# Optimization experiments

Hardware: AMD Instinct MI355X
Metric: run time of the kernel (lower is better)

## Reference

```python
import jax, jax.numpy as jnp
import numpy as np
from jax import lax

D = 8          # conv_out_size
HID = 128      # lstm hidden
EMB = 32       # word embed
GD = 256       # g/f mlp width


def _coords():
    # faithful to cvt_coord with python3 float division on first component
    c = np.zeros((D * D, 2), dtype=np.float32)
    for i in range(D * D):
        c[i, 0] = (i / D - D / 2) / (D / 2.0)
        c[i, 1] = (i % D - D / 2) / (D / 2.0)
    return jnp.asarray(c)


def _conv_bn(x, k, b, gamma, beta):
    y = lax.conv_general_dilated(x, k, (2, 2), [(1, 1), (1, 1)],
                                 dimension_numbers=('NCHW', 'OIHW', 'NCHW'))
    y = jax.nn.relu(y + b[None, :, None, None])
    m = y.mean((0, 2, 3))
    v = ((y - m[None, :, None, None]) ** 2).mean((0, 2, 3))  # biased var (train-mode BN)
    y = (y - m[None, :, None, None]) * lax.rsqrt(v + 1e-5)[None, :, None, None]
    return gamma[None, :, None, None] * y + beta[None, :, None, None]


def setup_inputs() -> dict:
    key = jax.random.key(0)
    ks = iter(jax.random.split(key, 48))
    B, T, QV, AV = 64, 18, 90, 28
    n = lambda sh, s=0.1: jax.random.normal(next(ks), sh, jnp.float32) * s
    inp = {
        'img': jax.random.normal(next(ks), (B, 3, 128, 128), jnp.float32),
        'qst_idxs': jax.random.randint(next(ks), (B, T), 0, QV),
        'emb': n((QV, EMB)).at[0].set(0.0),  # padding_idx=0
        'W_ih': n((4 * HID, EMB)), 'W_hh': n((4 * HID, HID)),
        'b_ih': n((4 * HID,)), 'b_hh': n((4 * HID,)),
        'k1': n((24, 3, 3, 3)), 'cb1': n((24,)), 'g1': jnp.ones((24,)), 'be1': jnp.zeros((24,)),
        'k2': n((24, 24, 3, 3)), 'cb2': n((24,)), 'g2': jnp.ones((24,)), 'be2': jnp.zeros((24,)),
        'k3': n((24, 24, 3, 3)), 'cb3': n((24,)), 'g3': jnp.ones((24,)), 'be3': jnp.zeros((24,)),
        'k4': n((24, 24, 3, 3)), 'cb4': n((24,)), 'g4': jnp.ones((24,)), 'be4': jnp.zeros((24,)),
        'Wg1': n((GD, 180)), 'bg1': n((GD,)),
        'Wg2': n((GD, GD)), 'bg2': n((GD,)),
        'Wg3': n((GD, GD)), 'bg3': n((GD,)),
        'Wg4': n((GD, GD)), 'bg4': n((GD,)),
        'Wf1': n((GD, GD)), 'bf1': n((GD,)),
        'Wf2': n((GD, GD)), 'bf2': n((GD,)),
        'Wf3': n((AV, GD)), 'bf3': n((AV,)),
        'h0': jax.random.normal(next(ks), (B, HID), jnp.float32),
        'c0': jax.random.normal(next(ks), (B, HID), jnp.float32),
    }
    return inp


def reference(img, qst_idxs, emb, W_ih, W_hh, b_ih, b_hh,
              k1, cb1, g1, be1, k2, cb2, g2, be2, k3, cb3, g3, be3, k4, cb4, g4, be4,
              Wg1, bg1, Wg2, bg2, Wg3, bg3, Wg4, bg4,
              Wf1, bf1, Wf2, bf2, Wf3, bf3, h0, c0):
    B = img.shape[0]
    # --- question encoder: embedding (padding_idx=0) + LSTM, take final CELL state ---
    we = emb[qst_idxs] * (qst_idxs != 0)[..., None].astype(emb.dtype)  # [B,T,32]

    def step(carry, x_t):
        h, c = carry
        gates = x_t @ W_ih.T + h @ W_hh.T + (b_ih + b_hh)
        i, f, g, o = jnp.split(gates, 4, axis=-1)
        c = jax.nn.sigmoid(f) * c + jax.nn.sigmoid(i) * jnp.tanh(g)
        h = jax.nn.sigmoid(o) * jnp.tanh(c)
        return (h, c), None

    (h_n, c_n), _ = lax.scan(step, (h0, c0), we.transpose(1, 0, 2))
    qst = c_n  # original uses self.hidden[1][-1] == cell state, [B,128]

    # --- conv stack ---
    x = _conv_bn(img, k1, cb1, g1, be1)
    x = _conv_bn(x, k2, cb2, g2, be2)
    x = _conv_bn(x, k3, cb3, g3, be3)
    x = _conv_bn(x, k4, cb4, g4, be4)  # [B,24,8,8]

    xf = x.reshape(B, 24, D * D).transpose(0, 2, 1)            # [B,64,24]
    xf = jnp.concatenate([xf, jnp.broadcast_to(_coords(), (B, D * D, 2))], 2)  # [B,64,26]

    # --- g-MLP over all pairs; first linear decomposed across x_i / x_j / qst ---
    # pair (k,j) feature = [x_flat[j](26), x_flat[k](26), qst(128)]
    Ai = xf @ Wg1[:, :26].T                    # [B,64,256], x_i part (index j)
    Aj = xf @ Wg1[:, 26:52].T                  # [B,64,256], x_j part (index k)
    Q = qst @ Wg1[:, 52:].T + bg1              # [B,256]
    h = jax.nn.relu(Ai[:, None, :, :] + Aj[:, :, None, :] + Q[:, None, None, :])  # [B,64,64,256]
    h = jax.nn.relu(h @ Wg2.T + bg2)
    h = jax.nn.relu(h @ Wg3.T + bg3)
    h = jax.nn.relu(h @ Wg4.T + bg4)
    xg = h.sum((1, 2))                          # [B,256] sum-pool over pairs

    # --- f-MLP (dropout = identity in eval) ---
    xfc = jax.nn.relu(xg @ Wf1.T + bf1)
    xfc = jax.nn.relu(xfc @ Wf2.T + bf2)
    logits = xfc @ Wf3.T + bf3
    return jax.nn.log_softmax(logits, axis=-1)
```

## Files before the change

### kernel.cpp

```cpp
#include <hip/hip_runtime.h>
#include <math.h>

typedef __bf16 bf16x8 __attribute__((ext_vector_type(8)));
typedef float  f32x16 __attribute__((ext_vector_type(16)));

#define DEVFN __device__ __forceinline__

DEVFN unsigned short f2bfh(float f) {
    __bf16 h = (__bf16)f;
    union { __bf16 h; unsigned short u; } v; v.h = h;
    return v.u;
}
DEVFN float sigmoidf_(float x) { return 1.0f / (1.0f + expf(-x)); }

__global__ void lstm_cvt_kernel(const int* __restrict__ qidx, const float* __restrict__ emb,
                                const float* __restrict__ Wih, const float* __restrict__ Whh,
                                const float* __restrict__ bih, const float* __restrict__ bhh,
                                const float* __restrict__ h0, const float* __restrict__ c0,
                                float* __restrict__ qst,
                                const float* __restrict__ Wg2, const float* __restrict__ Wg3,
                                const float* __restrict__ Wg4,
                                unsigned short* __restrict__ Wt2, unsigned short* __restrict__ Wt3,
                                unsigned short* __restrict__ Wt4)
{
    int tid = threadIdx.x;
    if (blockIdx.x >= 64) {
        int i = (blockIdx.x - 64) * 512 + tid;
        int seg = i >> 16, idx = i & 65535;
        const float* src = (seg == 0) ? Wg2 : (seg == 1) ? Wg3 : Wg4;
        unsigned short* dst = (seg == 0) ? Wt2 : (seg == 1) ? Wt3 : Wt4;
        int col = idx >> 8, k = idx & 255;
        dst[(k >> 3)*2048 + col*8 + (k & 7)] = f2bfh(src[idx]);
        return;
    }
    int b = blockIdx.x;
    __shared__ float hs[128], cs[128], xs[32], gs[512];
    if (tid < 128) { hs[tid] = h0[b*128 + tid]; cs[tid] = c0[b*128 + tid]; }
    float bsum = bih[tid] + bhh[tid];
    for (int t = 0; t < 18; ++t) {
        if (tid < 32) {
            int id = qidx[b*18 + t];
            xs[tid] = (id != 0) ? emb[id*32 + tid] : 0.0f;
        }
        __syncthreads();
        float g = bsum;
        const float* wi = Wih + tid*32;
        #pragma unroll
        for (int d = 0; d < 32; ++d) g += xs[d] * wi[d];
        const float* wh = Whh + tid*128;
        for (int d = 0; d < 128; ++d) g += hs[d] * wh[d];
        gs[tid] = g;
        __syncthreads();
        if (tid < 128) {
            float ig = sigmoidf_(gs[tid]);
            float fg = sigmoidf_(gs[128 + tid]);
            float gg = tanhf(gs[256 + tid]);
            float og = sigmoidf_(gs[384 + tid]);
            float cn = fg * cs[tid] + ig * gg;
            cs[tid] = cn;
            hs[tid] = og * tanhf(cn);
        }
        __syncthreads();
    }
    if (tid < 128) qst[b*128 + tid] = cs[tid];
}

__launch_bounds__(256, 4)
__global__ void conv1_kernel(const float* __restrict__ img, const float* __restrict__ wk,
                             const float* __restrict__ cb, float* __restrict__ y1)
{
    __shared__ float simg[3][9][128];
    __shared__ __align__(16) float wl[3][9][24];
    __shared__ float cbs[24];
    int b = blockIdx.x, t = blockIdx.y, tid = threadIdx.x;
    for (int i = tid; i < 648; i += 256) {
        int co = i / 27, rem = i % 27;
        wl[rem / 9][rem % 9][co] = wk[i];
    }
    if (tid < 24) cbs[tid] = cb[tid];
    int base = 8*t - 1;
    for (int i = tid; i < 3*9*128; i += 256) {
        int ci = i / (9*128); int r2 = i % (9*128);
        int row = r2 / 128, colx = r2 % 128;
        int ih = base + row;
        simg[ci][row][colx] = (ih >= 0 && ih < 128) ?
            img[((size_t)(b*3 + ci)*128 + ih)*128 + colx] : 0.f;
    }
    __syncthreads();

    int ow = tid & 63;
    int os = tid >> 6;
    int oh = t*4 + os;
    float* yb = y1 + ((size_t)b*24*64 + oh)*64 + ow;

    #pragma unroll
    for (int co4 = 0; co4 < 24; co4 += 4) {
        float a0 = 0.f, a1 = 0.f, a2 = 0.f, a3 = 0.f;
        #pragma unroll
        for (int ci = 0; ci < 3; ++ci)
          #pragma unroll
          for (int kh = 0; kh < 3; ++kh)
            #pragma unroll
            for (int kw = 0; kw < 3; ++kw) {
                int iw = ow*2 + kw - 1;
                float x = (iw >= 0 && iw < 128) ? simg[ci][2*os + kh][iw] : 0.f;
                float4 w4 = *reinterpret_cast<const float4*>(&wl[ci][kh*3 + kw][co4]);
                a0 += x*w4.x; a1 += x*w4.y; a2 += x*w4.z; a3 += x*w4.w;
            }
        yb[(size_t)(co4+0)*4096] = fmaxf(a0 + cbs[co4+0], 0.f);
        yb[(size_t)(co4+1)*4096] = fmaxf(a1 + cbs[co4+1], 0.f);
        yb[(size_t)(co4+2)*4096] = fmaxf(a2 + cbs[co4+2], 0.f);
        yb[(size_t)(co4+3)*4096] = fmaxf(a3 + cbs[co4+3], 0.f);
    }
}

__global__ void bn_partial_kernel(const float* __restrict__ y, float* __restrict__ part,
                                  int HW, int nb)
{
    int c = blockIdx.x;
    int s = blockIdx.y;
    int S = gridDim.y;
    int tid = threadIdx.x;
    int n4 = HW >> 2;
    float sum = 0.f, sum2 = 0.f;
    for (int b = s * nb; b < (s + 1) * nb; ++b) {
        const float4* p = reinterpret_cast<const float4*>(y + ((size_t)(b*24 + c)) * HW);
        for (int i = tid; i < n4; i += 256) {
            float4 v = p[i];
            sum  += v.x + v.y + v.z + v.w;
            sum2 += v.x*v.x + v.y*v.y + v.z*v.z + v.w*v.w;
        }
    }
    __shared__ float rs[256], rs2[256];
    rs[tid] = sum; rs2[tid] = sum2;
    __syncthreads();
    for (int st = 128; st > 0; st >>= 1) {
        if (tid < st) { rs[tid] += rs[tid + st]; rs2[tid] += rs2[tid + st]; }
        __syncthreads();
    }
    if (tid == 0) {
        part[(c * S + s) * 2]     = rs[0];
        part[(c * S + s) * 2 + 1] = rs2[0];
    }
}

#define BN_FOLD(bnp, gamma, beta, S, N, abs_, abo_, tid)                    \
    if (tid < 24) {                                                          \
        float s_ = 0.f, s2_ = 0.f;                                           \
        for (int i_ = 0; i_ < (S); ++i_) {                                   \
            s_  += (bnp)[((tid)*(S) + i_)*2];                                \
            s2_ += (bnp)[((tid)*(S) + i_)*2 + 1];                            \
        }                                                                    \
        float m_ = s_ / (N);                                                 \
        float v_ = s2_ / (N) - m_*m_;                                        \
        float r_ = rsqrtf(v_ + 1e-5f);                                       \
        float a_ = (gamma)[tid] * r_;                                        \
        (abs_)[tid] = a_; (abo_)[tid] = (beta)[tid] - m_*a_;                 \
    }

__launch_bounds__(128, 4)
__global__ void conv2_kernel(const float* __restrict__ y1, const float* __restrict__ wk,
                             const float* __restrict__ cb,
                             const float* __restrict__ bnp, const float* __restrict__ gamma,
                             const float* __restrict__ beta,
                             float* __restrict__ y2)
{
    __shared__ float sin2[24][5][64];
    __shared__ float wl[24][9][24];
    __shared__ float cbs[24];
    __shared__ float abs_[24], abo_[24];
    int b = blockIdx.x, t = blockIdx.y, tid = threadIdx.x;
    BN_FOLD(bnp, gamma, beta, 16, 262144, abs_, abo_, tid);
    for (int i = tid; i < 5184; i += 128) {
        int co = i / 216, rem = i % 216;
        int ci = rem / 9, tap = rem % 9;
        wl[ci][tap][co] = wk[i];
    }
    if (tid < 24) cbs[tid] = cb[tid];
    __syncthreads();
    int base = 4*t - 1;
    for (int i = tid; i < 24*5*64; i += 128) {
        int ci = i / (5*64); int r2 = i % (5*64);
        int row = r2 / 64, colx = r2 % 64;
        int ih = base + row;
        sin2[ci][row][colx] = (ih >= 0 && ih < 64) ?
            y1[((size_t)(b*24 + ci)*64 + ih)*64 + colx] * abs_[ci] + abo_[ci] : 0.f;
    }
    __syncthreads();

    int pos = tid & 63;
    int ow = pos & 31, os = pos >> 5;
    int ch = tid >> 6;
    int oh = 2*t + os;
    float acc[12];
    #pragma unroll
    for (int c = 0; c < 12; ++c) acc[c] = 0.f;

    for (int ci = 0; ci < 24; ++ci) {
        #pragma unroll
        for (int kh = 0; kh < 3; ++kh)
          #pragma unroll
          for (int kw = 0; kw < 3; ++kw) {
            int iw = ow*2 + kw - 1;
            float x = (iw >= 0 && iw < 64) ? sin2[ci][2*os + kh][iw] : 0.f;
            const float* wv = &wl[ci][kh*3 + kw][ch*12];
            #pragma unroll
            for (int c4 = 0; c4 < 3; ++c4) {
                float4 w4 = *reinterpret_cast<const float4*>(wv + c4*4);
                acc[c4*4+0] += x*w4.x;
                acc[c4*4+1] += x*w4.y;
                acc[c4*4+2] += x*w4.z;
                acc[c4*4+3] += x*w4.w;
            }
          }
    }
    #pragma unroll
    for (int c = 0; c < 12; ++c) {
        int co = ch*12 + c;
        y2[((size_t)(b*24 + co)*32 + oh)*32 + ow] = fmaxf(acc[c] + cbs[co], 0.f);
    }
}

__launch_bounds__(256, 2)
__global__ void conv_kernel(const float* __restrict__ in, const float* __restrict__ wk,
                            const float* __restrict__ cb,
                            const float* __restrict__ bnp, const float* __restrict__ gamma,
                            const float* __restrict__ beta, int S, int N,
                            float* __restrict__ out,
                            int Cin, int Hin, int Win, int Hout, int Wout)
{
    int cob = blockIdx.x;
    int co = cob % 24, b = cob / 24;
    int tid = threadIdx.x;
    __shared__ float sw[24*9];
    __shared__ float so9[9];
    __shared__ float bias;
    __shared__ float abs_[24], abo_[24];
    BN_FOLD(bnp, gamma, beta, S, N, abs_, abo_, tid);
    __syncthreads();
    if (tid < Cin*9) {
        int ci = tid / 9, t = tid % 9;
        sw[tid] = wk[(co*Cin + ci)*9 + t] * abs_[ci];
    }
    if (tid < 9) {
        float s = 0.f;
        for (int ci = 0; ci < Cin; ++ci)
            s += abo_[ci] * wk[(co*Cin + ci)*9 + tid];
        so9[tid] = s;
    }
    if (tid == 0) bias = cb[co];
    __syncthreads();

    int HW = Hout * Wout;
    int pos = tid;
    if (pos >= HW) return;
    int ow = pos % Wout, oh = pos / Wout;

    float acc = bias;
    #pragma unroll
    for (int kh = 0; kh < 3; ++kh) {
        int ih = oh*2 + kh - 1;
        bool vh = (ih >= 0 && ih < Hin);
        #pragma unroll
        for (int kw = 0; kw < 3; ++kw) {
            int iw = ow*2 + kw - 1;
            if (vh && iw >= 0 && iw < Win) acc += so9[kh*3 + kw];
        }
    }
    const float* ipb = in + ((size_t)b * Cin) * Hin * Win;
    for (int ci = 0; ci < Cin; ++ci) {
        const float* ip = ipb + (size_t)ci * Hin * Win;
        const float* swp = sw + ci*9;
        #pragma unroll
        for (int kh = 0; kh < 3; ++kh) {
            int ih = oh*2 + kh - 1;
            if (ih < 0 || ih >= Hin) continue;
            #pragma unroll
            for (int kw = 0; kw < 3; ++kw) {
                int iw = ow*2 + kw - 1;
                if (iw < 0 || iw >= Win) continue;
                acc += ip[ih*Win + iw] * swp[kh*3 + kw];
            }
        }
    }
    out[((size_t)(b*24 + co)) * HW + pos] = fmaxf(acc, 0.0f);
}

__global__ void aiajq_kernel(const float* __restrict__ y4,
                             const float* __restrict__ bnp, const float* __restrict__ gamma,
                             const float* __restrict__ beta,
                             const float* __restrict__ qst,
                             const float* __restrict__ Wg1, const float* __restrict__ bg1,
                             float* __restrict__ Ai, float* __restrict__ Aj, float* __restrict__ Q)
{
    int b = blockIdx.x, c = threadIdx.x;
    __shared__ float xfl[64 * 26];
    __shared__ float qv[128];
    __shared__ float abs_[24], abo_[24];
    BN_FOLD(bnp, gamma, beta, 1, 4096, abs_, abo_, c);
    __syncthreads();
    for (int i = c; i < 64*24; i += 256) {
        int p = i / 24, ch = i % 24;
        xfl[p*26 + ch] = y4[((size_t)(b*24 + ch)) * 64 + p] * abs_[ch] + abo_[ch];
    }
    if (c < 64) {
        xfl[c*26 + 24] = ((float)c / 8.0f - 4.0f) * 0.25f;
        xfl[c*26 + 25] = ((float)(c % 8) - 4.0f) * 0.25f;
    }
    if (c < 128) qv[c] = qst[b*128 + c];
    __syncthreads();
    const float* w = Wg1 + (size_t)c * 180;
    float wa[26], wb[26];
    #pragma unroll
    for (int d = 0; d < 26; ++d) { wa[d] = w[d]; wb[d] = w[26 + d]; }
    float q = bg1[c];
    for (int d = 0; d < 128; ++d) q += qv[d] * w[52 + d];
    Q[b*256 + c] = q;
    for (int j = 0; j < 64; ++j) {
        const float* xr = xfl + j*26;
        float sa = 0.f, sb = 0.f;
        #pragma unroll
        for (int d = 0; d < 26; ++d) { sa += xr[d]*wa[d]; sb += xr[d]*wb[d]; }
        Ai[((size_t)(b*64 + j))*256 + c] = sa;
        Aj[((size_t)(b*64 + j))*256 + c] = sb;
    }
}

__launch_bounds__(512, 4)
__global__ void gmlp_kernel(const float* __restrict__ Ai, const float* __restrict__ Aj,
                            const float* __restrict__ Q,
                            const unsigned short* __restrict__ Wt2, const float* __restrict__ bg2,
                            const unsigned short* __restrict__ Wt3, const float* __restrict__ bg3,
                            const unsigned short* __restrict__ Wt4, const float* __restrict__ bg4,
                            float* __restrict__ partial)
{
    constexpr int LDP = 264;
    __shared__ __align__(16) unsigned short buf[128 * LDP];
    int tid = threadIdx.x;
    int blk = blockIdx.x;
    int b = blk >> 5;
    int k0 = (blk & 31) << 1;

    {
        int g  = tid >> 8;
        int jh = (tid >> 7) & 1;
        int c2 = tid & 127;
        float2 aj = *((const float2*)(Aj + ((size_t)(b*64 + k0 + g))*256) + c2);
        float2 qq = *((const float2*)(Q + b*256) + c2);
        float a0 = aj.x + qq.x, a1 = aj.y + qq.y;
        const float2* aip = (const float2*)(Ai + ((size_t)b*64)*256) + c2;
        #pragma unroll 4
        for (int j = jh*32; j < jh*32 + 32; ++j) {
            float2 av = aip[(size_t)j*128];
            unsigned lo = f2bfh(fmaxf(av.x + a0, 0.f));
            unsigned hv = f2bfh(fmaxf(av.y + a1, 0.f));
            *(unsigned*)(&buf[(size_t)(g*64 + j)*LDP + 2*c2]) = lo | (hv << 16);
        }
    }
    __syncthreads();

    int l = tid & 63, w = tid >> 6;
    int rh = w >> 2;
    int cg = w & 3;
    int lid = l & 31, hi = l >> 5;
    int arow = rh*64 + lid;
    int colA = cg*64 + lid;
    int colB = colA + 32;

    const unsigned short* Ws[3] = {Wt2, Wt3, Wt4};
    const float* Bs[3] = {bg2, bg3, bg4};

    #pragma unroll
    for (int layer = 0; layer < 3; ++layer) {
        const unsigned short* W = Ws[layer];
        const float* bias = Bs[layer];
        f32x16 acc00, acc01, acc10, acc11;
        #pragma unroll
        for (int i = 0; i < 16; ++i) { acc00[i]=0.f; acc01[i]=0.f; acc10[i]=0.f; acc11[i]=0.f; }

        const unsigned short* wp0 = W + (size_t)hi*2048 + colA*8;
        const unsigned short* wp1 = W + (size_t)hi*2048 + colB*8;
        const unsigned short* ap  = buf + arow*LDP + hi*8;

        #pragma unroll
        for (int kk = 0; kk < 16; ++kk) {
            bf16x8 b0 = *reinterpret_cast<const bf16x8*>(wp0 + kk*4096);
            bf16x8 b1 = *reinterpret_cast<const bf16x8*>(wp1 + kk*4096);
            bf16x8 a0 = *reinterpret_cast<const bf16x8*>(ap + kk*16);
            bf16x8 a1 = *reinterpret_cast<const bf16x8*>(ap + 32*LDP + kk*16);
            acc00 = __builtin_amdgcn_mfma_f32_32x32x16_bf16(a0, b0, acc00, 0, 0, 0);
            acc01 = __builtin_amdgcn_mfma_f32_32x32x16_bf16(a0, b1, acc01, 0, 0, 0);
            acc10 = __builtin_amdgcn_mfma_f32_32x32x16_bf16(a1, b0, acc10, 0, 0, 0);
            acc11 = __builtin_amdgcn_mfma_f32_32x32x16_bf16(a1, b1, acc11, 0, 0, 0);
        }

        if (layer < 2) {
            float bc0 = bias[colA], bc1 = bias[colB];
            __syncthreads();
            #pragma unroll
            for (int reg = 0; reg < 16; ++reg) {
                int r0 = rh*64 + (reg & 3) + 8*(reg >> 2) + 4*hi;
                buf[r0*LDP + colA] = f2bfh(fmaxf(acc00[reg] + bc0, 0.f));
                buf[r0*LDP + colB] = f2bfh(fmaxf(acc01[reg] + bc1, 0.f));
                int r1 = r0 + 32;
                buf[r1*LDP + colA] = f2bfh(fmaxf(acc10[reg] + bc0, 0.f));
                buf[r1*LDP + colB] = f2bfh(fmaxf(acc11[reg] + bc1, 0.f));
            }
            __syncthreads();
        } else {
            float bc0 = bias[colA], bc1 = bias[colB];
            float cs0 = 0.f, cs1 = 0.f;
            #pragma unroll
            for (int reg = 0; reg < 16; ++reg) {
                cs0 += fmaxf(acc00[reg] + bc0, 0.f) + fmaxf(acc10[reg] + bc0, 0.f);
                cs1 += fmaxf(acc01[reg] + bc1, 0.f) + fmaxf(acc11[reg] + bc1, 0.f);
            }
            cs0 += __shfl_xor(cs0, 32);
            cs1 += __shfl_xor(cs1, 32);
            if (hi == 0) {
                float* pp = partial + ((size_t)blk*2 + rh)*256;
                pp[colA] = cs0;
                pp[colB] = cs1;
            }
        }
    }
}

__global__ void fmlp_kernel(const float* __restrict__ partial,
                            const float* __restrict__ Wf1, const float* __restrict__ bf1,
                            const float* __restrict__ Wf2, const float* __restrict__ bf2,
                            const float* __restrict__ Wf3, const float* __restrict__ bf3,
                            float* __restrict__ out)
{
    int b = blockIdx.x, tid = threadIdx.x;
    __shared__ float v0[256], v1[256], lgt[28];
    {
        float s0 = 0.f, s1 = 0.f, s2 = 0.f, s3 = 0.f;
        const float* p = partial + ((size_t)b * 64) * 256 + tid;
        #pragma unroll
        for (int k = 0; k < 64; k += 4) {
            s0 += p[(size_t)(k+0) * 256];
            s1 += p[(size_t)(k+1) * 256];
            s2 += p[(size_t)(k+2) * 256];
            s3 += p[(size_t)(k+3) * 256];
        }
        v0[tid] = (s0 + s1) + (s2 + s3);
    }
    __syncthreads();
    {
        float s = bf1[tid];
        const float4* wr = reinterpret_cast<const float4*>(Wf1 + (size_t)tid * 256);
        for (int k4 = 0; k4 < 64; ++k4) {
            float4 wv = wr[k4];
            s += wv.x*v0[k4*4+0] + wv.y*v0[k4*4+1] + wv.z*v0[k4*4+2] + wv.w*v0[k4*4+3];
        }
        v1[tid] = fmaxf(s, 0.f);
    }
    __syncthreads();
    {
        float s = bf2[tid];
        const float4* wr = reinterpret_cast<const float4*>(Wf2 + (size_t)tid * 256);
        for (int k4 = 0; k4 < 64; ++k4) {
            float4 wv = wr[k4];
            s += wv.x*v1[k4*4+0] + wv.y*v1[k4*4+1] + wv.z*v1[k4*4+2] + wv.w*v1[k4*4+3];
        }
        v0[tid] = fmaxf(s, 0.f);
    }
    __syncthreads();
    if (tid < 28) {
        float s = bf3[tid];
        const float4* wr = reinterpret_cast<const float4*>(Wf3 + (size_t)tid * 256);
        for (int k4 = 0; k4 < 64; ++k4) {
            float4 wv = wr[k4];
            s += wv.x*v0[k4*4+0] + wv.y*v0[k4*4+1] + wv.z*v0[k4*4+2] + wv.w*v0[k4*4+3];
        }
        lgt[tid] = s;
    }
    __syncthreads();
    if (tid == 0) {
        float mx = -1e30f;
        for (int i = 0; i < 28; ++i) mx = fmaxf(mx, lgt[i]);
        float se = 0.f;
        for (int i = 0; i < 28; ++i) se += expf(lgt[i] - mx);
        float lse = mx + logf(se);
        for (int i = 0; i < 28; ++i) out[b*28 + i] = lgt[i] - lse;
    }
}

extern "C" void kernel_launch(void* const* d_in, const int* in_sizes, int n_in,
                              void* d_out, int out_size, void* d_ws, size_t ws_size,
                              hipStream_t stream)
{
    (void)in_sizes; (void)n_in; (void)out_size; (void)ws_size;
    const float* img = (const float*)d_in[0];
    const int*   qidx= (const int*)  d_in[1];
    const float* emb = (const float*)d_in[2];
    const float* Wih = (const float*)d_in[3];
    const float* Whh = (const float*)d_in[4];
    const float* bih = (const float*)d_in[5];
    const float* bhh = (const float*)d_in[6];
    const float* k1  = (const float*)d_in[7];  const float* cb1=(const float*)d_in[8];
    const float* g1  = (const float*)d_in[9];  const float* be1=(const float*)d_in[10];
    const float* k2  = (const float*)d_in[11]; const float* cb2=(const float*)d_in[12];
    const float* g2  = (const float*)d_in[13]; const float* be2=(const float*)d_in[14];
    const float* k3  = (const float*)d_in[15]; const float* cb3=(const float*)d_in[16];
    const float* g3  = (const float*)d_in[17]; const float* be3=(const float*)d_in[18];
    const float* k4  = (const float*)d_in[19]; const float* cb4=(const float*)d_in[20];
    const float* g4  = (const float*)d_in[21]; const float* be4=(const float*)d_in[22];
    const float* Wg1 = (const float*)d_in[23]; const float* bg1=(const float*)d_in[24];
    const float* Wg2 = (const float*)d_in[25]; const float* bg2=(const float*)d_in[26];
    const float* Wg3 = (const float*)d_in[27]; const float* bg3=(const float*)d_in[28];
    const float* Wg4 = (const float*)d_in[29]; const float* bg4=(const float*)d_in[30];
    const float* Wf1 = (const float*)d_in[31]; const float* bf1=(const float*)d_in[32];
    const float* Wf2 = (const float*)d_in[33]; const float* bf2=(const float*)d_in[34];
    const float* Wf3 = (const float*)d_in[35]; const float* bf3=(const float*)d_in[36];
    const float* h0  = (const float*)d_in[37]; const float* c0 =(const float*)d_in[38];
    float* out = (float*)d_out;

    float* ws = (float*)d_ws;
    float* y1 = ws;   ws += 64*24*64*64;
    float* y2 = ws;   ws += 64*24*32*32;
    float* y3 = ws;   ws += 64*24*16*16;
    float* y4 = ws;   ws += 64*24*8*8;
    float* bnp = ws;  ws += 24*16*2;
    float* qst = ws;  ws += 64*128;
    float* Ai  = ws;  ws += 64*64*256;
    float* Aj  = ws;  ws += 64*64*256;
    float* Qb  = ws;  ws += 64*256;
    unsigned short* Wt2 = (unsigned short*)ws; ws += 65536/2;
    unsigned short* Wt3 = (unsigned short*)ws; ws += 65536/2;
    unsigned short* Wt4 = (unsigned short*)ws; ws += 65536/2;
    float* partial = ws; ws += 2048*2*256;

    lstm_cvt_kernel<<<448, 512, 0, stream>>>(qidx, emb, Wih, Whh, bih, bhh, h0, c0, qst,
                                             Wg2, Wg3, Wg4, Wt2, Wt3, Wt4);

    conv1_kernel<<<dim3(64, 16), 256, 0, stream>>>(img, k1, cb1, y1);
    bn_partial_kernel<<<dim3(24,16), 256, 0, stream>>>(y1, bnp, 64*64, 4);
    conv2_kernel<<<dim3(64, 16), 128, 0, stream>>>(y1, k2, cb2, bnp, g1, be1, y2);
    bn_partial_kernel<<<dim3(24,8), 256, 0, stream>>>(y2, bnp, 32*32, 8);
    conv_kernel<<<dim3(64*24, 1), 256, 0, stream>>>(y2, k3, cb3, bnp, g2, be2, 8, 64*32*32,
                                                    y3, 24, 32, 32, 16, 16);
    bn_partial_kernel<<<dim3(24,4), 256, 0, stream>>>(y3, bnp, 16*16, 16);
    conv_kernel<<<dim3(64*24, 1), 256, 0, stream>>>(y3, k4, cb4, bnp, g3, be3, 4, 64*16*16,
                                                    y4, 24, 16, 16, 8, 8);
    bn_partial_kernel<<<dim3(24,1), 256, 0, stream>>>(y4, bnp, 8*8, 64);

    aiajq_kernel<<<64, 256, 0, stream>>>(y4, bnp, g4, be4, qst, Wg1, bg1, Ai, Aj, Qb);

    gmlp_kernel<<<2048, 512, 0, stream>>>(Ai, Aj, Qb, Wt2, bg2, Wt3, bg3, Wt4, bg4, partial);
    fmlp_kernel<<<64, 256, 0, stream>>>(partial, Wf1, bf1, Wf2, bf2, Wf3, bf3, out);
}
```

Baseline: 474.1 us.

## Fuse conv/BN/AiAjQ pipeline into one persistent kernel with grid barriers

```diff
diff --git a/kernel.cpp b/kernel.cpp
--- a/kernel.cpp
+++ b/kernel.cpp
@@ -12,6 +12,36 @@
     return v.u;
 }
 DEVFN float sigmoidf_(float x) { return 1.0f / (1.0f + expf(-x)); }
+
+DEVFN void gsync(unsigned* cnt, unsigned* gen, unsigned nb, unsigned target) {
+    __syncthreads();
+    if (threadIdx.x == 0) {
+        __threadfence();
+        if (atomicAdd(cnt, 1u) == nb - 1u) {
+            atomicExch(cnt, 0u);
+            __threadfence();
+            atomicExch(gen, target);
+        } else {
+            while (atomicAdd(gen, 0u) < target) __builtin_amdgcn_s_sleep(2);
+        }
+        __threadfence();
+    }
+    __syncthreads();
+}
+
+#define BN_FOLD(bnp, gamma, beta, S, N, abs_, abo_, tid)                    \
+    if (tid < 24) {                                                          \
+        float s_ = 0.f, s2_ = 0.f;                                           \
+        for (int i_ = 0; i_ < (S); ++i_) {                                   \
+            s_  += (bnp)[((tid)*(S) + i_)*2];                                \
+            s2_ += (bnp)[((tid)*(S) + i_)*2 + 1];                            \
+        }                                                                    \
+        float m_ = s_ / (N);                                                 \
+        float v_ = s2_ / (N) - m_*m_;                                        \
+        float r_ = rsqrtf(v_ + 1e-5f);                                       \
+        float a_ = (gamma)[tid] * r_;                                        \
+        (abs_)[tid] = a_; (abo_)[tid] = (beta)[tid] - m_*a_;                 \
+    }
 
 __global__ void lstm_cvt_kernel(const int* __restrict__ qidx, const float* __restrict__ emb,
                                 const float* __restrict__ Wih, const float* __restrict__ Whh,
@@ -65,264 +95,373 @@
     if (tid < 128) qst[b*128 + tid] = cs[tid];
 }
 
-__launch_bounds__(256, 4)
-__global__ void conv1_kernel(const float* __restrict__ img, const float* __restrict__ wk,
-                             const float* __restrict__ cb, float* __restrict__ y1)
+__launch_bounds__(256, 3)
+__global__ void mega_kernel(const float* __restrict__ img,
+                            const float* __restrict__ k1, const float* __restrict__ cb1,
+                            const float* __restrict__ g1, const float* __restrict__ be1,
+                            const float* __restrict__ k2, const float* __restrict__ cb2,
+                            const float* __restrict__ g2, const float* __restrict__ be2,
+                            const float* __restrict__ k3, const float* __restrict__ cb3,
+                            const float* __restrict__ g3, const float* __restrict__ be3,
+                            const float* __restrict__ k4, const float* __restrict__ cb4,
+                            const float* __restrict__ g4, const float* __restrict__ be4,
+                            const float* __restrict__ qst,
+                            const float* __restrict__ Wg1, const float* __restrict__ bg1,
+                            float* __restrict__ y1, float* __restrict__ y2,
+                            float* __restrict__ y3, float* __restrict__ y4,
+                            float* __restrict__ bnp1, float* __restrict__ bnp2,
+                            float* __restrict__ bnp3, float* __restrict__ bnp4,
+                            float* __restrict__ Ai, float* __restrict__ Aj, float* __restrict__ Q,
+                            unsigned* __restrict__ bar)
 {
-    __shared__ float simg[3][9][128];
-    __shared__ __align__(16) float wl[3][9][24];
-    __shared__ float cbs[24];
-    int b = blockIdx.x, t = blockIdx.y, tid = threadIdx.x;
-    for (int i = tid; i < 648; i += 256) {
-        int co = i / 27, rem = i % 27;
-        wl[rem / 9][rem % 9][co] = wk[i];
-    }
-    if (tid < 24) cbs[tid] = cb[tid];
-    int base = 8*t - 1;
-    for (int i = tid; i < 3*9*128; i += 256) {
-        int ci = i / (9*128); int r2 = i % (9*128);
-        int row = r2 / 128, colx = r2 % 128;
-        int ih = base + row;
-        simg[ci][row][colx] = (ih >= 0 && ih < 128) ?
-            img[((size_t)(b*3 + ci)*128 + ih)*128 + colx] : 0.f;
-    }
-    __syncthreads();
-
-    int ow = tid & 63;
-    int os = tid >> 6;
-    int oh = t*4 + os;
-    float* yb = y1 + ((size_t)b*24*64 + oh)*64 + ow;
-
-    #pragma unroll
-    for (int co4 = 0; co4 < 24; co4 += 4) {
-        float a0 = 0.f, a1 = 0.f, a2 = 0.f, a3 = 0.f;
-        #pragma unroll
-        for (int ci = 0; ci < 3; ++ci)
-          #pragma unroll
-          for (int kh = 0; kh < 3; ++kh)
+    __shared__ __align__(16) float smem[12936];
+    const int tid = threadIdx.x;
+    const int blk = blockIdx.x;
+    const unsigned NB = 512;
+    unsigned* cnt = bar;
+    unsigned* gen = bar + 1;
+
+    {
+        float* simg = smem;
+        float* wl   = smem + 3456;
+        float* cbs  = smem + 4104;
+        for (int i = tid; i < 648; i += 256) {
+            int co = i / 27, rem = i % 27;
+            wl[((rem / 9) * 9 + (rem % 9)) * 24 + co] = k1[i];
+        }
+        if (tid < 24) cbs[tid] = cb1[tid];
+        #pragma unroll
+        for (int it = 0; it < 2; ++it) {
+            int u = blk + it * 512;
+            int b = u >> 4, t = u & 15;
+            __syncthreads();
+            int base = 8 * t - 1;
+            for (int i = tid; i < 3 * 9 * 128; i += 256) {
+                int ci = i / 1152; int r2 = i % 1152;
+                int row = r2 >> 7, colx = r2 & 127;
+                int ih = base + row;
+                simg[ci * 1152 + row * 128 + colx] = (ih >= 0 && ih < 128) ?
+                    img[((size_t)(b * 3 + ci) * 128 + ih) * 128 + colx] : 0.f;
+            }
+            __syncthreads();
+            int ow = tid & 63;
+            int os = tid >> 6;
+            int oh = t * 4 + os;
+            float* yb = y1 + ((size_t)b * 24 * 64 + oh) * 64 + ow;
             #pragma unroll
-            for (int kw = 0; kw < 3; ++kw) {
-                int iw = ow*2 + kw - 1;
-                float x = (iw >= 0 && iw < 128) ? simg[ci][2*os + kh][iw] : 0.f;
-                float4 w4 = *reinterpret_cast<const float4*>(&wl[ci][kh*3 + kw][co4]);
-                a0 += x*w4.x; a1 += x*w4.y; a2 += x*w4.z; a3 += x*w4.w;
-            }
-        yb[(size_t)(co4+0)*4096] = fmaxf(a0 + cbs[co4+0], 0.f);
-        yb[(size_t)(co4+1)*4096] = fmaxf(a1 + cbs[co4+1], 0.f);
-        yb[(size_t)(co4+2)*4096] = fmaxf(a2 + cbs[co4+2], 0.f);
-        yb[(size_t)(co4+3)*4096] = fmaxf(a3 + cbs[co4+3], 0.f);
-    }
-}
-
-__global__ void bn_partial_kernel(const float* __restrict__ y, float* __restrict__ part,
-                                  int HW, int nb)
-{
-    int c = blockIdx.x;
-    int s = blockIdx.y;
-    int S = gridDim.y;
-    int tid = threadIdx.x;
-    int n4 = HW >> 2;
-    float sum = 0.f, sum2 = 0.f;
-    for (int b = s * nb; b < (s + 1) * nb; ++b) {
-        const float4* p = reinterpret_cast<const float4*>(y + ((size_t)(b*24 + c)) * HW);
-        for (int i = tid; i < n4; i += 256) {
-            float4 v = p[i];
-            sum  += v.x + v.y + v.z + v.w;
-            sum2 += v.x*v.x + v.y*v.y + v.z*v.z + v.w*v.w;
-        }
-    }
-    __shared__ float rs[256], rs2[256];
-    rs[tid] = sum; rs2[tid] = sum2;
-    __syncthreads();
-    for (int st = 128; st > 0; st >>= 1) {
-        if (tid < st) { rs[tid] += rs[tid + st]; rs2[tid] += rs2[tid + st]; }
-        __syncthreads();
-    }
-    if (tid == 0) {
-        part[(c * S + s) * 2]     = rs[0];
-        part[(c * S + s) * 2 + 1] = rs2[0];
-    }
-}
-
-#define BN_FOLD(bnp, gamma, beta, S, N, abs_, abo_, tid)                    \
-    if (tid < 24) {                                                          \
-        float s_ = 0.f, s2_ = 0.f;                                           \
-        for (int i_ = 0; i_ < (S); ++i_) {                                   \
-            s_  += (bnp)[((tid)*(S) + i_)*2];                                \
-            s2_ += (bnp)[((tid)*(S) + i_)*2 + 1];                            \
-        }                                                                    \
-        float m_ = s_ / (N);                                                 \
-        float v_ = s2_ / (N) - m_*m_;                                        \
-        float r_ = rsqrtf(v_ + 1e-5f);                                       \
-        float a_ = (gamma)[tid] * r_;                                        \
-        (abs_)[tid] = a_; (abo_)[tid] = (beta)[tid] - m_*a_;                 \
-    }
-
-__launch_bounds__(128, 4)
-__global__ void conv2_kernel(const float* __restrict__ y1, const float* __restrict__ wk,
-                             const float* __restrict__ cb,
-                             const float* __restrict__ bnp, const float* __restrict__ gamma,
-                             const float* __restrict__ beta,
-                             float* __restrict__ y2)
-{
-    __shared__ float sin2[24][5][64];
-    __shared__ float wl[24][9][24];
-    __shared__ float cbs[24];
-    __shared__ float abs_[24], abo_[24];
-    int b = blockIdx.x, t = blockIdx.y, tid = threadIdx.x;
-    BN_FOLD(bnp, gamma, beta, 16, 262144, abs_, abo_, tid);
-    for (int i = tid; i < 5184; i += 128) {
-        int co = i / 216, rem = i % 216;
-        int ci = rem / 9, tap = rem % 9;
-        wl[ci][tap][co] = wk[i];
-    }
-    if (tid < 24) cbs[tid] = cb[tid];
-    __syncthreads();
-    int base = 4*t - 1;
-    for (int i = tid; i < 24*5*64; i += 128) {
-        int ci = i / (5*64); int r2 = i % (5*64);
-        int row = r2 / 64, colx = r2 % 64;
-        int ih = base + row;
-        sin2[ci][row][colx] = (ih >= 0 && ih < 64) ?
-            y1[((size_t)(b*24 + ci)*64 + ih)*64 + colx] * abs_[ci] + abo_[ci] : 0.f;
-    }
-    __syncthreads();
-
-    int pos = tid & 63;
-    int ow = pos & 31, os = pos >> 5;
-    int ch = tid >> 6;
-    int oh = 2*t + os;
-    float acc[12];
-    #pragma unroll
-    for (int c = 0; c < 12; ++c) acc[c] = 0.f;
-
-    for (int ci = 0; ci < 24; ++ci) {
-        #pragma unroll
-        for (int kh = 0; kh < 3; ++kh)
-          #pragma unroll
-          for (int kw = 0; kw < 3; ++kw) {
-            int iw = ow*2 + kw - 1;
-            float x = (iw >= 0 && iw < 64) ? sin2[ci][2*os + kh][iw] : 0.f;
-            const float* wv = &wl[ci][kh*3 + kw][ch*12];
+            for (int co4 = 0; co4 < 24; co4 += 4) {
+                float a0 = 0.f, a1 = 0.f, a2 = 0.f, a3 = 0.f;
+                #pragma unroll
+                for (int ci = 0; ci < 3; ++ci)
+                  #pragma unroll
+                  for (int kh = 0; kh < 3; ++kh)
+                    #pragma unroll
+                    for (int kw = 0; kw < 3; ++kw) {
+                        int iw = ow * 2 + kw - 1;
+                        float x = (iw >= 0 && iw < 128) ?
+                            simg[ci * 1152 + (2 * os + kh) * 128 + iw] : 0.f;
+                        float4 w4 = *reinterpret_cast<const float4*>(
+                            &wl[(ci * 9 + kh * 3 + kw) * 24 + co4]);
+                        a0 += x * w4.x; a1 += x * w4.y; a2 += x * w4.z; a3 += x * w4.w;
+                    }
+                yb[(size_t)(co4 + 0) * 4096] = fmaxf(a0 + cbs[co4 + 0], 0.f);
+                yb[(size_t)(co4 + 1) * 4096] = fmaxf(a1 + cbs[co4 + 1], 0.f);
+                yb[(size_t)(co4 + 2) * 4096] = fmaxf(a2 + cbs[co4 + 2], 0.f);
+                yb[(size_t)(co4 + 3) * 4096] = fmaxf(a3 + cbs[co4 + 3], 0.f);
+            }
+        }
+    }
+    gsync(cnt, gen, NB, 1);
+
+    if (blk < 384) {
+        int c = blk >> 4, s = blk & 15;
+        float sum = 0.f, sum2 = 0.f;
+        for (int b = s * 4; b < s * 4 + 4; ++b) {
+            const float4* p = reinterpret_cast<const float4*>(y1 + ((size_t)(b * 24 + c)) * 4096);
+            for (int i = tid; i < 1024; i += 256) {
+                float4 v = p[i];
+                sum  += v.x + v.y + v.z + v.w;
+                sum2 += v.x * v.x + v.y * v.y + v.z * v.z + v.w * v.w;
+            }
+        }
+        float* rs = smem; float* rs2 = smem + 256;
+        rs[tid] = sum; rs2[tid] = sum2;
+        __syncthreads();
+        for (int st = 128; st > 0; st >>= 1) {
+            if (tid < st) { rs[tid] += rs[tid + st]; rs2[tid] += rs2[tid + st]; }
+            __syncthreads();
+        }
+        if (tid == 0) { bnp1[(c * 16 + s) * 2] = rs[0]; bnp1[(c * 16 + s) * 2 + 1] = rs2[0]; }
+    }
+    gsync(cnt, gen, NB, 2);
+
+    {
+        float* sin2 = smem;
+        float* wl   = smem + 7680;
+        float* cbs  = smem + 12864;
+        float* abs_ = smem + 12888;
+        float* abo_ = smem + 12912;
+        BN_FOLD(bnp1, g1, be1, 16, 262144, abs_, abo_, tid);
+        for (int i = tid; i < 5184; i += 256) {
+            int co = i / 216, rem = i % 216;
+            wl[rem * 24 + co] = k2[i];
+        }
+        if (tid < 24) cbs[tid] = cb2[tid];
+        #pragma unroll
+        for (int it = 0; it < 2; ++it) {
+            int u = blk + it * 512;
+            int b = u >> 4, t = u & 15;
+            __syncthreads();
+            int base = 4 * t - 1;
+            for (int i = tid; i < 7680; i += 256) {
+                int ci = i / 320; int r2 = i % 320;
+                int row = r2 >> 6, colx = r2 & 63;
+                int ih = base + row;
+                sin2[ci * 320 + row * 64 + colx] = (ih >= 0 && ih < 64) ?
+                    y1[((size_t)(b * 24 + ci) * 64 + ih) * 64 + colx] * abs_[ci] + abo_[ci] : 0.f;
+            }
+            __syncthreads();
+            int pos = tid & 63;
+            int ow = pos & 31, os = pos >> 5;
+            int ch = tid >> 6;
+            int oh = 2 * t + os;
+            float a0 = 0.f, a1 = 0.f, a2 = 0.f, a3 = 0.f, a4 = 0.f, a5 = 0.f;
+            for (int ci = 0; ci < 24; ++ci) {
+                #pragma unroll
+                for (int kh = 0; kh < 3; ++kh)
+                  #pragma unroll
+                  for (int kw = 0; kw < 3; ++kw) {
+                      int iw = ow * 2 + kw - 1;
+                      float x = (iw >= 0 && iw < 64) ?
+                          sin2[ci * 320 + (2 * os + kh) * 64 + iw] : 0.f;
+                      const float* wv = &wl[(ci * 9 + kh * 3 + kw) * 24 + ch * 6];
+                      float2 w0 = *reinterpret_cast<const float2*>(wv);
+                      float2 w1 = *reinterpret_cast<const float2*>(wv + 2);
+                      float2 w2 = *reinterpret_cast<const float2*>(wv + 4);
+                      a0 += x * w0.x; a1 += x * w0.y;
+                      a2 += x * w1.x; a3 += x * w1.y;
+                      a4 += x * w2.x; a5 += x * w2.y;
+                  }
+            }
+            float* ob = y2 + ((size_t)(b * 24 + ch * 6) * 32 + oh) * 32 + ow;
+            ob[0]            = fmaxf(a0 + cbs[ch * 6 + 0], 0.f);
+            ob[(size_t)1024] = fmaxf(a1 + cbs[ch * 6 + 1], 0.f);
+            ob[(size_t)2048] = fmaxf(a2 + cbs[ch * 6 + 2], 0.f);
+            ob[(size_t)3072] = fmaxf(a3 + cbs[ch * 6 + 3], 0.f);
+            ob[(size_t)4096] = fmaxf(a4 + cbs[ch * 6 + 4], 0.f);
+            ob[(size_t)5120] = fmaxf(a5 + cbs[ch * 6 + 5], 0.f);
+        }
+    }
+    gsync(cnt, gen, NB, 3);
+
+    if (blk < 192) {
+        int c = blk >> 3, s = blk & 7;
+        float sum = 0.f, sum2 = 0.f;
+        for (int b = s * 8; b < s * 8 + 8; ++b) {
+            const float4* p = reinterpret_cast<const float4*>(y2 + ((size_t)(b * 24 + c)) * 1024);
+            for (int i = tid; i < 256; i += 256) {
+                float4 v = p[i];
+                sum  += v.x + v.y + v.z + v.w;
+                sum2 += v.x * v.x + v.y * v.y + v.z * v.z + v.w * v.w;
+            }
+        }
+        float* rs = smem; float* rs2 = smem + 256;
+        rs[tid] = sum; rs2[tid] = sum2;
+        __syncthreads();
+        for (int st = 128; st > 0; st >>= 1) {
+            if (tid < st) { rs[tid] += rs[tid + st]; rs2[tid] += rs2[tid + st]; }
+            __syncthreads();
+        }
+        if (tid == 0) { bnp2[(c * 8 + s) * 2] = rs[0]; bnp2[(c * 8 + s) * 2 + 1] = rs2[0]; }
+    }
+    gsync(cnt, gen, NB, 4);
+
+    {
+        float* abs_ = smem;
+        float* abo_ = smem + 24;
+        float* sw   = smem + 48;
+        float* so9  = smem + 264;
+        float* bias = smem + 273;
+        BN_FOLD(bnp2, g2, be2, 8, 65536, abs_, abo_, tid);
+        #pragma unroll
+        for (int it = 0; it < 3; ++it) {
+            int u = blk + it * 512;
+            int co = u % 24, b = u / 24;
+            __syncthreads();
+            if (tid < 216) {
+                int ci = tid / 9, tp = tid % 9;
+                sw[tid] = k3[(co * 24 + ci) * 9 + tp] * abs_[ci];
+            }
+            if (tid < 9) {
+                float s = 0.f;
+                for (int ci = 0; ci < 24; ++ci) s += abo_[ci] * k3[(co * 24 + ci) * 9 + tid];
+                so9[tid] = s;
+            }
+            if (tid == 0) bias[0] = cb3[co];
+            __syncthreads();
+            int ow = tid & 15, oh = tid >> 4;
+            float acc = bias[0];
             #pragma unroll
-            for (int c4 = 0; c4 < 3; ++c4) {
-                float4 w4 = *reinterpret_cast<const float4*>(wv + c4*4);
-                acc[c4*4+0] += x*w4.x;
-                acc[c4*4+1] += x*w4.y;
-                acc[c4*4+2] += x*w4.z;
-                acc[c4*4+3] += x*w4.w;
-            }
-          }
-    }
-    #pragma unroll
-    for (int c = 0; c < 12; ++c) {
-        int co = ch*12 + c;
-        y2[((size_t)(b*24 + co)*32 + oh)*32 + ow] = fmaxf(acc[c] + cbs[co], 0.f);
-    }
-}
-
-__launch_bounds__(256, 2)
-__global__ void conv_kernel(const float* __restrict__ in, const float* __restrict__ wk,
-                            const float* __restrict__ cb,
-                            const float* __restrict__ bnp, const float* __restrict__ gamma,
-                            const float* __restrict__ beta, int S, int N,
-                            float* __restrict__ out,
-                            int Cin, int Hin, int Win, int Hout, int Wout)
-{
-    int cob = blockIdx.x;
-    int co = cob % 24, b = cob / 24;
-    int tid = threadIdx.x;
-    __shared__ float sw[24*9];
-    __shared__ float so9[9];
-    __shared__ float bias;
-    __shared__ float abs_[24], abo_[24];
-    BN_FOLD(bnp, gamma, beta, S, N, abs_, abo_, tid);
-    __syncthreads();
-    if (tid < Cin*9) {
-        int ci = tid / 9, t = tid % 9;
-        sw[tid] = wk[(co*Cin + ci)*9 + t] * abs_[ci];
-    }
-    if (tid < 9) {
-        float s = 0.f;
-        for (int ci = 0; ci < Cin; ++ci)
-            s += abo_[ci] * wk[(co*Cin + ci)*9 + tid];
-        so9[tid] = s;
-    }
-    if (tid == 0) bias = cb[co];
-    __syncthreads();
-
-    int HW = Hout * Wout;
-    int pos = tid;
-    if (pos >= HW) return;
-    int ow = pos % Wout, oh = pos / Wout;
-
-    float acc = bias;
-    #pragma unroll
-    for (int kh = 0; kh < 3; ++kh) {
-        int ih = oh*2 + kh - 1;
-        bool vh = (ih >= 0 && ih < Hin);
-        #pragma unroll
-        for (int kw = 0; kw < 3; ++kw) {
-            int iw = ow*2 + kw - 1;
-            if (vh && iw >= 0 && iw < Win) acc += so9[kh*3 + kw];
-        }
-    }
-    const float* ipb = in + ((size_t)b * Cin) * Hin * Win;
-    for (int ci = 0; ci < Cin; ++ci) {
-        const float* ip = ipb + (size_t)ci * Hin * Win;
-        const float* swp = sw + ci*9;
-        #pragma unroll
-        for (int kh = 0; kh < 3; ++kh) {
-            int ih = oh*2 + kh - 1;
-            if (ih < 0 || ih >= Hin) continue;
+            for (int kh = 0; kh < 3; ++kh) {
+                int ih = oh * 2 + kh - 1;
+                bool vh = (ih >= 0 && ih < 32);
+                #pragma unroll
+                for (int kw = 0; kw < 3; ++kw) {
+                    int iw = ow * 2 + kw - 1;
+                    if (vh && iw >= 0 && iw < 32) acc += so9[kh * 3 + kw];
+                }
+            }
+            const float* ipb = y2 + ((size_t)b * 24) * 1024;
+            for (int ci = 0; ci < 24; ++ci) {
+                const float* ip = ipb + (size_t)ci * 1024;
+                const float* swp = sw + ci * 9;
+                #pragma unroll
+                for (int kh = 0; kh < 3; ++kh) {
+                    int ih = oh * 2 + kh - 1;
+                    if (ih < 0 || ih >= 32) continue;
+                    #pragma unroll
+                    for (int kw = 0; kw < 3; ++kw) {
+                        int iw = ow * 2 + kw - 1;
+                        if (iw < 0 || iw >= 32) continue;
+                        acc += ip[ih * 32 + iw] * swp[kh * 3 + kw];
+                    }
+                }
+            }
+            y3[((size_t)(b * 24 + co)) * 256 + tid] = fmaxf(acc, 0.f);
+        }
+    }
+    gsync(cnt, gen, NB, 5);
+
+    if (blk < 96) {
+        int c = blk >> 2, s = blk & 3;
+        float sum = 0.f, sum2 = 0.f;
+        for (int b = s * 16; b < s * 16 + 16; ++b) {
+            const float4* p = reinterpret_cast<const float4*>(y3 + ((size_t)(b * 24 + c)) * 256);
+            for (int i = tid; i < 64; i += 256) {
+                float4 v = p[i];
+                sum  += v.x + v.y + v.z + v.w;
+                sum2 += v.x * v.x + v.y * v.y + v.z * v.z + v.w * v.w;
+            }
+        }
+        float* rs = smem; float* rs2 = smem + 256;
+        rs[tid] = sum; rs2[tid] = sum2;
+        __syncthreads();
+        for (int st = 128; st > 0; st >>= 1) {
+            if (tid < st) { rs[tid] += rs[tid + st]; rs2[tid] += rs2[tid + st]; }
+            __syncthreads();
+        }
+        if (tid == 0) { bnp3[(c * 4 + s) * 2] = rs[0]; bnp3[(c * 4 + s) * 2 + 1] = rs2[0]; }
+    }
+    gsync(cnt, gen, NB, 6);
+
+    if (blk < 64) {
+        float* ytile = smem;
+        float* wl    = smem + 6144;
+        float* cbs   = smem + 11328;
+        float* abs_  = smem + 11352;
+        float* abo_  = smem + 11376;
+        int b = blk;
+        BN_FOLD(bnp3, g3, be3, 4, 16384, abs_, abo_, tid);
+        for (int i = tid; i < 5184; i += 256) {
+            int co = i / 216, rem = i % 216;
+            wl[rem * 24 + co] = k4[i];
+        }
+        if (tid < 24) cbs[tid] = cb4[tid];
+        __syncthreads();
+        for (int i = tid; i < 6144; i += 256) {
+            int ci = i >> 8, p = i & 255;
+            ytile[i] = y3[((size_t)(b * 24 + ci)) * 256 + p] * abs_[ci] + abo_[ci];
+        }
+        __syncthreads();
+        int pos = tid & 63;
+        int ow = pos & 7, oh = pos >> 3;
+        int cg = tid >> 6;
+        float a0 = 0.f, a1 = 0.f, a2 = 0.f, a3 = 0.f, a4 = 0.f, a5 = 0.f;
+        for (int ci = 0; ci < 24; ++ci) {
             #pragma unroll
-            for (int kw = 0; kw < 3; ++kw) {
-                int iw = ow*2 + kw - 1;
-                if (iw < 0 || iw >= Win) continue;
-                acc += ip[ih*Win + iw] * swp[kh*3 + kw];
-            }
-        }
-    }
-    out[((size_t)(b*24 + co)) * HW + pos] = fmaxf(acc, 0.0f);
-}
-
-__global__ void aiajq_kernel(const float* __restrict__ y4,
-                             const float* __restrict__ bnp, const float* __restrict__ gamma,
-                             const float* __restrict__ beta,
-                             const float* __restrict__ qst,
-                             const float* __restrict__ Wg1, const float* __restrict__ bg1,
-                             float* __restrict__ Ai, float* __restrict__ Aj, float* __restrict__ Q)
-{
-    int b = blockIdx.x, c = threadIdx.x;
-    __shared__ float xfl[64 * 26];
-    __shared__ float qv[128];
-    __shared__ float abs_[24], abo_[24];
-    BN_FOLD(bnp, gamma, beta, 1, 4096, abs_, abo_, c);
-    __syncthreads();
-    for (int i = c; i < 64*24; i += 256) {
-        int p = i / 24, ch = i % 24;
-        xfl[p*26 + ch] = y4[((size_t)(b*24 + ch)) * 64 + p] * abs_[ch] + abo_[ch];
-    }
-    if (c < 64) {
-        xfl[c*26 + 24] = ((float)c / 8.0f - 4.0f) * 0.25f;
-        xfl[c*26 + 25] = ((float)(c % 8) - 4.0f) * 0.25f;
-    }
-    if (c < 128) qv[c] = qst[b*128 + c];
-    __syncthreads();
-    const float* w = Wg1 + (size_t)c * 180;
-    float wa[26], wb[26];
-    #pragma unroll
-    for (int d = 0; d < 26; ++d) { wa[d] = w[d]; wb[d] = w[26 + d]; }
-    float q = bg1[c];
-    for (int d = 0; d < 128; ++d) q += qv[d] * w[52 + d];
-    Q[b*256 + c] = q;
-    for (int j = 0; j < 64; ++j) {
-        const float* xr = xfl + j*26;
-        float sa = 0.f, sb = 0.f;
-        #pragma unroll
-        for (int d = 0; d < 26; ++d) { sa += xr[d]*wa[d]; sb += xr[d]*wb[d]; }
-        Ai[((size_t)(b*64 + j))*256 + c] = sa;
-        Aj[((size_t)(b*64 + j))*256 + c] = sb;
+            for (int kh = 0; kh < 3; ++kh) {
+                int ih = oh * 2 + kh - 1;
+                if (ih < 0 || ih >= 16) continue;
+                #pragma unroll
+                for (int kw = 0; kw < 3; ++kw) {
+                    int iw = ow * 2 + kw - 1;
+                    if (iw < 0 || iw >= 16) continue;
+                    float x = ytile[ci * 256 + ih * 16 + iw];
+                    const float* wv = &wl[(ci * 9 + kh * 3 + kw) * 24 + cg * 6];
+                    float2 w0 = *reinterpret_cast<const float2*>(wv);
+                    float2 w1 = *reinterpret_cast<const float2*>(wv + 2);
+                    float2 w2 = *reinterpret_cast<const float2*>(wv + 4);
+                    a0 += x * w0.x; a1 += x * w0.y;
+                    a2 += x * w1.x; a3 += x * w1.y;
+                    a4 += x * w2.x; a5 += x * w2.y;
+                }
+            }
+        }
+        float* ob = y4 + ((size_t)(b * 24 + cg * 6)) * 64 + pos;
+        ob[0]          = fmaxf(a0 + cbs[cg * 6 + 0], 0.f);
+        ob[(size_t)64] = fmaxf(a1 + cbs[cg * 6 + 1], 0.f);
+        ob[(size_t)128]= fmaxf(a2 + cbs[cg * 6 + 2], 0.f);
+        ob[(size_t)192]= fmaxf(a3 + cbs[cg * 6 + 3], 0.f);
+        ob[(size_t)256]= fmaxf(a4 + cbs[cg * 6 + 4], 0.f);
+        ob[(size_t)320]= fmaxf(a5 + cbs[cg * 6 + 5], 0.f);
+    }
+    gsync(cnt, gen, NB, 7);
+
+    if (blk < 24) {
+        int c = blk;
+        float sum = 0.f, sum2 = 0.f;
+        for (int b = 0; b < 64; ++b) {
+            const float4* p = reinterpret_cast<const float4*>(y4 + ((size_t)(b * 24 + c)) * 64);
+            for (int i = tid; i < 16; i += 256) {
+                float4 v = p[i];
+                sum  += v.x + v.y + v.z + v.w;
+                sum2 += v.x * v.x + v.y * v.y + v.z * v.z + v.w * v.w;
+            }
+        }
+        float* rs = smem; float* rs2 = smem + 256;
+        rs[tid] = sum; rs2[tid] = sum2;
+        __syncthreads();
+        for (int st = 128; st > 0; st >>= 1) {
+            if (tid < st) { rs[tid] += rs[tid + st]; rs2[tid] += rs2[tid + st]; }
+            __syncthreads();
+        }
+        if (tid == 0) { bnp4[c * 2] = rs[0]; bnp4[c * 2 + 1] = rs2[0]; }
+    }
+    gsync(cnt, gen, NB, 8);
+
+    if (blk < 64) {
+        float* xfl  = smem;
+        float* qv   = smem + 1664;
+        float* abs_ = smem + 1792;
+        float* abo_ = smem + 1816;
+        int b = blk, c = tid;
+        BN_FOLD(bnp4, g4, be4, 1, 4096, abs_, abo_, c);
+        __syncthreads();
+        for (int i = c; i < 64 * 24; i += 256) {
+            int p = i / 24, ch = i % 24;
+            xfl[p * 26 + ch] = y4[((size_t)(b * 24 + ch)) * 64 + p] * abs_[ch] + abo_[ch];
+        }
+        if (c < 64) {
+            xfl[c * 26 + 24] = ((float)c / 8.0f - 4.0f) * 0.25f;
+            xfl[c * 26 + 25] = ((float)(c % 8) - 4.0f) * 0.25f;
+        }
+        if (c < 128) qv[c] = qst[b * 128 + c];
+        __syncthreads();
+        const float* w = Wg1 + (size_t)c * 180;
+        float wa[26], wb[26];
+        #pragma unroll
+        for (int d = 0; d < 26; ++d) { wa[d] = w[d]; wb[d] = w[26 + d]; }
+        float q = bg1[c];
+        for (int d = 0; d < 128; ++d) q += qv[d] * w[52 + d];
+        Q[b * 256 + c] = q;
+        for (int j = 0; j < 64; ++j) {
+            const float* xr = xfl + j * 26;
+            float sa = 0.f, sb = 0.f;
+            #pragma unroll
+            for (int d = 0; d < 26; ++d) { sa += xr[d] * wa[d]; sb += xr[d] * wb[d]; }
+            Ai[((size_t)(b * 64 + j)) * 256 + c] = sa;
+            Aj[((size_t)(b * 64 + j)) * 256 + c] = sb;
+        }
     }
 }
 
@@ -522,7 +661,10 @@
     float* y2 = ws;   ws += 64*24*32*32;
     float* y3 = ws;   ws += 64*24*16*16;
     float* y4 = ws;   ws += 64*24*8*8;
-    float* bnp = ws;  ws += 24*16*2;
+    float* bnp1 = ws; ws += 24*16*2;
+    float* bnp2 = ws; ws += 24*8*2;
+    float* bnp3 = ws; ws += 24*4*2;
+    float* bnp4 = ws; ws += 24*2;
     float* qst = ws;  ws += 64*128;
     float* Ai  = ws;  ws += 64*64*256;
     float* Aj  = ws;  ws += 64*64*256;
@@ -531,22 +673,17 @@
     unsigned short* Wt3 = (unsigned short*)ws; ws += 65536/2;
     unsigned short* Wt4 = (unsigned short*)ws; ws += 65536/2;
     float* partial = ws; ws += 2048*2*256;
+    unsigned* bar = (unsigned*)ws; ws += 4;
+
+    hipMemsetAsync(bar, 0, 16, stream);
 
     lstm_cvt_kernel<<<448, 512, 0, stream>>>(qidx, emb, Wih, Whh, bih, bhh, h0, c0, qst,
                                              Wg2, Wg3, Wg4, Wt2, Wt3, Wt4);
 
-    conv1_kernel<<<dim3(64, 16), 256, 0, stream>>>(img, k1, cb1, y1);
-    bn_partial_kernel<<<dim3(24,16), 256, 0, stream>>>(y1, bnp, 64*64, 4);
-    conv2_kernel<<<dim3(64, 16), 128, 0, stream>>>(y1, k2, cb2, bnp, g1, be1, y2);
-    bn_partial_kernel<<<dim3(24,8), 256, 0, stream>>>(y2, bnp, 32*32, 8);
-    conv_kernel<<<dim3(64*24, 1), 256, 0, stream>>>(y2, k3, cb3, bnp, g2, be2, 8, 64*32*32,
-                                                    y3, 24, 32, 32, 16, 16);
-    bn_partial_kernel<<<dim3(24,4), 256, 0, stream>>>(y3, bnp, 16*16, 16);
-    conv_kernel<<<dim3(64*24, 1), 256, 0, stream>>>(y3, k4, cb4, bnp, g3, be3, 4, 64*16*16,
-                                                    y4, 24, 16, 16, 8, 8);
-    bn_partial_kernel<<<dim3(24,1), 256, 0, stream>>>(y4, bnp, 8*8, 64);
-
-    aiajq_kernel<<<64, 256, 0, stream>>>(y4, bnp, g4, be4, qst, Wg1, bg1, Ai, Aj, Qb);
+    mega_kernel<<<512, 256, 0, stream>>>(img, k1, cb1, g1, be1, k2, cb2, g2, be2,
+                                         k3, cb3, g3, be3, k4, cb4, g4, be4,
+                                         qst, Wg1, bg1, y1, y2, y3, y4,
+                                         bnp1, bnp2, bnp3, bnp4, Ai, Aj, Qb, bar);
 
     gmlp_kernel<<<2048, 512, 0, stream>>>(Ai, Aj, Qb, Wt2, bg2, Wt3, bg3, Wt4, bg4, partial);
     fmlp_kernel<<<64, 256, 0, stream>>>(partial, Wf1, bf1, Wf2, bf2, Wf3, bf3, out);
```

Result: slower. 752.4 us (+58.7%).
